# Performance work log

Hardware: AMD Instinct MI355X
Metric: run time of the kernel (lower is better)

Reference implementation:

```python
import jax, jax.numpy as jnp
import numpy as np

B, S, H, NH = 8, 1024, 1024, 16
HD = H // NH  # 64


def setup_inputs() -> dict:
    key = jax.random.key(0)
    ks = jax.random.split(key, 7)
    scale = 1.0 / np.sqrt(H)
    return {
        "hidden_states": jax.random.normal(ks[0], (B, S, H), jnp.float32),
        "Wq": jax.random.normal(ks[1], (H, H), jnp.float32) * scale,
        "bq": jax.random.normal(ks[2], (H,), jnp.float32) * 0.01,
        "Wk": jax.random.normal(ks[3], (H, H), jnp.float32) * scale,
        "bk": jax.random.normal(ks[4], (H,), jnp.float32) * 0.01,
        "Wv": jax.random.normal(ks[5], (H, H), jnp.float32) * scale,
        "bv": jax.random.normal(ks[6], (H,), jnp.float32) * 0.01,
    }


def _split_heads(x):
    # [B, S, H] -> [B, NH, S, HD]
    b, s, _ = x.shape
    return x.reshape(b, s, NH, HD).transpose(0, 2, 1, 3)


def reference(hidden_states, Wq, bq, Wk, bk, Wv, bv):
    q = _split_heads(hidden_states @ Wq.T + bq)
    k = _split_heads(hidden_states @ Wk.T + bk)
    v = _split_heads(hidden_states @ Wv.T + bv)
    scale = 1.0 / np.sqrt(HD).astype(np.float32)
    # [B, NH, S, S] attention logits (module materializes this fully)
    scores = jnp.einsum('bhld,bhsd->bhls', q, k) * scale
    probs = jax.nn.softmax(scores, axis=-1)  # dropout_p=0.0 -> no dropout
    ctx = jnp.einsum('bhls,bhsd->bhld', probs, v)
    # [B, NH, S, HD] -> [B, S, H]
    ctx = ctx.transpose(0, 2, 1, 3).reshape(hidden_states.shape[0], hidden_states.shape[1], H)
    return ctx
```

## Files before the change

### kernel.cpp

```cpp
#include <hip/hip_runtime.h>
#include <hip/hip_bf16.h>
#include <stdint.h>

#define B_  8
#define S_  1024
#define H_  1024
#define NH_ 16
#define HD_ 64
#define M_  (B_*S_)

using bf16x8 = __attribute__((ext_vector_type(8))) __bf16;
using f32x4  = __attribute__((ext_vector_type(4))) float;
using f32x16 = __attribute__((ext_vector_type(16))) float;
typedef int iv2 __attribute__((ext_vector_type(2)));

#define LOG2E 1.4426950408889634f

#if __has_builtin(__builtin_amdgcn_exp2f)
#define EXP2(x) __builtin_amdgcn_exp2f(x)
#else
#define EXP2(x) exp2f(x)
#endif

__device__ __forceinline__ void gload_lds16(const void* g, void* l) {
  __builtin_amdgcn_global_load_lds(
      (const __attribute__((address_space(1))) unsigned int*)g,
      (__attribute__((address_space(3))) unsigned int*)l, 16, 0, 0);
}

__device__ __forceinline__ unsigned pack_bf16(float lo, float hi) {
  unsigned r;
  asm("v_cvt_pk_bf16_f32 %0, %1, %2" : "=v"(r) : "v"(lo), "v"(hi));
  return r;
}

__device__ __forceinline__ void swapl32(unsigned& a, unsigned& b) {
#if __has_builtin(__builtin_amdgcn_permlane32_swap)
  iv2 r = __builtin_amdgcn_permlane32_swap((int)a, (int)b, false, false);
  a = (unsigned)r[0];
  b = (unsigned)r[1];
#else
  unsigned axc = (unsigned)__shfl_xor((int)a, 32);
  unsigned bxc = (unsigned)__shfl_xor((int)b, 32);
  int lane = threadIdx.x & 63;
  unsigned an = (lane < 32) ? a : bxc;
  unsigned bn = (lane < 32) ? axc : b;
  a = an; b = bn;
#endif
}

__global__ void __launch_bounds__(256) cast_bf16_kernel(const float* __restrict__ in,
                                                        __bf16* __restrict__ out, int n8) {
  int i = blockIdx.x * blockDim.x + threadIdx.x;
  int stride = gridDim.x * blockDim.x;
  for (; i < n8; i += stride) {
    float4 f0 = ((const float4*)in)[2 * i];
    float4 f1 = ((const float4*)in)[2 * i + 1];
    bf16x8 o;
    o[0] = (__bf16)f0.x; o[1] = (__bf16)f0.y; o[2] = (__bf16)f0.z; o[3] = (__bf16)f0.w;
    o[4] = (__bf16)f1.x; o[5] = (__bf16)f1.y; o[6] = (__bf16)f1.z; o[7] = (__bf16)f1.w;
    ((bf16x8*)out)[i] = o;
  }
}

__global__ void __launch_bounds__(256) qkv_gemm_kernel(
    const __bf16* __restrict__ X,
    const __bf16* __restrict__ Wq, const __bf16* __restrict__ Wk, const __bf16* __restrict__ Wv,
    const float* __restrict__ bq, const float* __restrict__ bk, const float* __restrict__ bv,
    __bf16* __restrict__ Qo, __bf16* __restrict__ Ko, __bf16* __restrict__ Vto) {
  __shared__ __align__(16) char Asm[128 * 128];
  __shared__ __align__(16) char Bsm[128 * 128];

  const int tid = threadIdx.x;
  const int lane = tid & 63, w = tid >> 6;
  const int l15 = lane & 15, g = lane >> 4;
  const int wr = w >> 1, wc = w & 1;
  const int m0 = blockIdx.x * 128;
  const int n0 = blockIdx.y * 128;
  const int z = blockIdx.z;
  const __bf16* W = (z == 0) ? Wq : ((z == 1) ? Wk : Wv);
  const float* bias = (z == 0) ? bq : ((z == 1) ? bk : bv);

  f32x4 acc[4][4] = {};

  for (int kt = 0; kt < H_; kt += 64) {
    __syncthreads();
#pragma unroll
    for (int is = 0; is < 4; ++is) {
      int q = is * 4096 + tid * 16;
      int row = q >> 7;
      int inrow = (q & 127) ^ ((row & 7) << 4);
      const char* ga = (const char*)X + (size_t)(m0 + row) * (H_ * 2) + kt * 2 + inrow;
      const char* gb = (const char*)W + (size_t)(n0 + row) * (H_ * 2) + kt * 2 + inrow;
      gload_lds16(ga, Asm + is * 4096 + w * 1024);
      gload_lds16(gb, Bsm + is * 4096 + w * 1024);
    }
    __syncthreads();
#pragma unroll
    for (int ks = 0; ks < 2; ++ks) {
      bf16x8 a[4], b[4];
#pragma unroll
      for (int i = 0; i < 4; ++i) {
        int row = wr * 64 + i * 16 + l15;
        int chunk = (g + ks * 4) ^ (row & 7);
        a[i] = *reinterpret_cast<const bf16x8*>(Asm + row * 128 + chunk * 16);
      }
#pragma unroll
      for (int j = 0; j < 4; ++j) {
        int row = wc * 64 + j * 16 + l15;
        int chunk = (g + ks * 4) ^ (row & 7);
        b[j] = *reinterpret_cast<const bf16x8*>(Bsm + row * 128 + chunk * 16);
      }
#pragma unroll
      for (int i = 0; i < 4; ++i)
#pragma unroll
        for (int j = 0; j < 4; ++j)
          acc[i][j] = __builtin_amdgcn_mfma_f32_16x16x32_bf16(a[i], b[j], acc[i][j], 0, 0, 0);
    }
  }

#pragma unroll
  for (int i = 0; i < 4; ++i) {
#pragma unroll
    for (int j = 0; j < 4; ++j) {
      int n = n0 + wc * 64 + j * 16 + l15;
      float bs = bias[n];
      int nh = n >> 6, d = n & 63;
#pragma unroll
      for (int r = 0; r < 4; ++r) {
        int m = m0 + wr * 64 + i * 16 + 4 * g + r;
        int bb = m >> 10, s = m & 1023;
        float v = acc[i][j][r] + bs;
        if (z == 0) {
          Qo[(((size_t)bb * NH_ + nh) * S_ + s) * HD_ + d] = (__bf16)(v * (0.125f * LOG2E));
        } else if (z == 1) {
          Ko[(((size_t)bb * NH_ + nh) * S_ + s) * HD_ + d] = (__bf16)v;
        } else {
          Vto[(((size_t)bb * NH_ + nh) * HD_ + d) * S_ + s] = (__bf16)v;
        }
      }
    }
  }
}

#define CROW(r, hi) (((r) & 3) + 8 * ((r) >> 2) + 4 * (hi))

__global__ void __launch_bounds__(512) attn_kernel(
    const __bf16* __restrict__ Q,
    const __bf16* __restrict__ K,
    const __bf16* __restrict__ Vt,
    float* __restrict__ Out) {
  __shared__ __align__(16) char Ksm[8192];
  __shared__ __align__(16) char Vsm[8192];
  __shared__ __align__(16) float stat_lds[512];

  const int tid = threadIdx.x, lane = tid & 63, w = tid >> 6;
  const int l31 = lane & 31, hi = lane >> 5;
  const int head = blockIdx.y;
  const int bb = head >> 4, nh = head & 15;
  const int qw = blockIdx.x * 256 + w * 32;

  const char* Qh = (const char*)(Q + (size_t)head * S_ * HD_);
  const char* Kh = (const char*)(K + (size_t)head * S_ * HD_);
  const char* Vh = (const char*)(Vt + (size_t)head * S_ * HD_);

  bf16x8 qf[4];
#pragma unroll
  for (int slot = 0; slot < 4; ++slot)
    qf[slot] = *reinterpret_cast<const bf16x8*>(
        Qh + (size_t)(qw + l31) * 128 + slot * 32 + hi * 16);

  float m_run = -1e30f, l_run = 0.0f;
  f32x16 accO[2] = {};

  for (int kv = 0; kv < S_; kv += 64) {
    __syncthreads();
    {
      int q = tid * 16;
      int row = q >> 7;
      int inrow = (q & 127) ^ ((row & 7) << 4);
      gload_lds16(Kh + (size_t)(kv + row) * 128 + inrow, Ksm + w * 1024);
      gload_lds16(Vh + (size_t)row * 2048 + kv * 2 + inrow, Vsm + w * 1024);
    }
    __syncthreads();

    f32x16 s0 = {}, s1 = {};
#pragma unroll
    for (int slot = 0; slot < 4; ++slot) {
      int c0 = slot * 2 + hi;
      int r0 = l31;
      bf16x8 k0 = *reinterpret_cast<const bf16x8*>(Ksm + r0 * 128 + ((c0 ^ (r0 & 7)) << 4));
      int r1 = 32 + l31;
      bf16x8 k1 = *reinterpret_cast<const bf16x8*>(Ksm + r1 * 128 + ((c0 ^ (r1 & 7)) << 4));
      s0 = __builtin_amdgcn_mfma_f32_32x32x16_bf16(k0, qf[slot], s0, 0, 0, 0);
      s1 = __builtin_amdgcn_mfma_f32_32x32x16_bf16(k1, qf[slot], s1, 0, 0, 0);
    }

    float mx = -1e30f;
#pragma unroll
    for (int r = 0; r < 16; ++r) mx = fmaxf(mx, fmaxf(s0[r], s1[r]));
    mx = fmaxf(mx, __shfl_xor(mx, 32));
    float mnew = fmaxf(m_run, mx);
    float corr = EXP2(m_run - mnew);
    float sum = 0.0f;
#pragma unroll
    for (int r = 0; r < 16; ++r) {
      float p0 = EXP2(s0[r] - mnew); s0[r] = p0; sum += p0;
      float p1 = EXP2(s1[r] - mnew); s1[r] = p1; sum += p1;
    }
    sum += __shfl_xor(sum, 32);
    l_run = l_run * corr + sum;
    m_run = mnew;

    stat_lds[w * 64 + lane] = corr;
    f32x4 c4[4];
#pragma unroll
    for (int rq = 0; rq < 4; ++rq)
      c4[rq] = *reinterpret_cast<const f32x4*>(&stat_lds[w * 64 + rq * 8 + hi * 4]);
#pragma unroll
    for (int r = 0; r < 16; ++r) {
      float cr = c4[r >> 2][r & 3];
      accO[0][r] *= cr;
      accO[1][r] *= cr;
    }

    bf16x8 pa[4];
#define BUILD_PA(T, rb)                                                     \
    {                                                                       \
      unsigned x1 = pack_bf16(T[rb + 0], T[rb + 1]);                        \
      unsigned x2 = pack_bf16(T[rb + 2], T[rb + 3]);                        \
      unsigned y1 = pack_bf16(T[rb + 4], T[rb + 5]);                        \
      unsigned y2 = pack_bf16(T[rb + 6], T[rb + 7]);                        \
      swapl32(x1, y1);                                                      \
      swapl32(x2, y2);                                                      \
      union { unsigned u[4]; bf16x8 v; } cvt;                               \
      cvt.u[0] = x1; cvt.u[1] = x2; cvt.u[2] = y1; cvt.u[3] = y2;           \
      pa_out = cvt.v;                                                       \
    }
    {
      bf16x8 pa_out;
      BUILD_PA(s0, 0) pa[0] = pa_out;
      BUILD_PA(s0, 8) pa[1] = pa_out;
      BUILD_PA(s1, 0) pa[2] = pa_out;
      BUILD_PA(s1, 8) pa[3] = pa_out;
    }

#pragma unroll
    for (int ks = 0; ks < 4; ++ks) {
#pragma unroll
      for (int dt = 0; dt < 2; ++dt) {
        int rd = dt * 32 + l31;
        int ck = ks * 2 + hi;
        bf16x8 vb = *reinterpret_cast<const bf16x8*>(Vsm + rd * 128 + ((ck ^ (rd & 7)) << 4));
        accO[dt] = __builtin_amdgcn_mfma_f32_32x32x16_bf16(pa[ks], vb, accO[dt], 0, 0, 0);
      }
    }
  }

  stat_lds[w * 64 + lane] = 1.0f / l_run;
  f32x4 li4[4];
#pragma unroll
  for (int rq = 0; rq < 4; ++rq)
    li4[rq] = *reinterpret_cast<const f32x4*>(&stat_lds[w * 64 + rq * 8 + hi * 4]);

  float* Ob = Out + (size_t)bb * S_ * H_ + (size_t)nh * HD_;
#pragma unroll
  for (int r = 0; r < 16; ++r) {
    int qabs = qw + CROW(r, hi);
    float li = li4[r >> 2][r & 3];
#pragma unroll
    for (int dt = 0; dt < 2; ++dt) {
      int d = dt * 32 + l31;
      Ob[(size_t)qabs * H_ + d] = accO[dt][r] * li;
    }
  }
}

extern "C" void kernel_launch(void* const* d_in, const int* in_sizes, int n_in,
                              void* d_out, int out_size, void* d_ws, size_t ws_size,
                              hipStream_t stream) {
  const float* hs = (const float*)d_in[0];
  const float* Wq = (const float*)d_in[1];
  const float* bq = (const float*)d_in[2];
  const float* Wk = (const float*)d_in[3];
  const float* bk = (const float*)d_in[4];
  const float* Wv = (const float*)d_in[5];
  const float* bv = (const float*)d_in[6];
  float* out = (float*)d_out;
  char* ws = (char*)d_ws;

  size_t off = 0;
  __bf16* Xb  = (__bf16*)(ws + off); off += (size_t)M_ * H_ * 2;
  __bf16* Wqb = (__bf16*)(ws + off); off += (size_t)H_ * H_ * 2;
  __bf16* Wkb = (__bf16*)(ws + off); off += (size_t)H_ * H_ * 2;
  __bf16* Wvb = (__bf16*)(ws + off); off += (size_t)H_ * H_ * 2;
  __bf16* Qb  = (__bf16*)(ws + off); off += (size_t)M_ * H_ * 2;
  __bf16* Kb  = (__bf16*)(ws + off); off += (size_t)M_ * H_ * 2;
  __bf16* Vtb = (__bf16*)(ws + off); off += (size_t)M_ * H_ * 2;

  cast_bf16_kernel<<<4096, 256, 0, stream>>>(hs, Xb, M_ * H_ / 8);
  cast_bf16_kernel<<<512, 256, 0, stream>>>(Wq, Wqb, H_ * H_ / 8);
  cast_bf16_kernel<<<512, 256, 0, stream>>>(Wk, Wkb, H_ * H_ / 8);
  cast_bf16_kernel<<<512, 256, 0, stream>>>(Wv, Wvb, H_ * H_ / 8);

  qkv_gemm_kernel<<<dim3(M_ / 128, H_ / 128, 3), 256, 0, stream>>>(
      Xb, Wqb, Wkb, Wvb, bq, bk, bv, Qb, Kb, Vtb);

  attn_kernel<<<dim3(S_ / 256, B_ * NH_), 512, 0, stream>>>(Qb, Kb, Vtb, out);
}
```

Measured before the change: 160.1 us.

## Rewrite QKV GEMM with 256x256 tiles and 4-stage LDS pipeline

Replaces the 128x128 synchronous QKV GEMM with 256x256 block tiles on 512 threads, a 4-slot LDS ring prefetching three K-tiles ahead with explicit vmcnt waits, interleaved half-tile MFMA phases with setprio, and an XCD-aware block swizzle. The goal is to hide global-load latency and raise arithmetic intensity and L2 reuse. In exchange it uses 128KB of dynamic LDS and many accumulator registers, which limits occupancy, and it depends on hand-placed waitcnt and barrier logic being correct.

```diff
diff --git a/kernel.cpp b/kernel.cpp
--- a/kernel.cpp
+++ b/kernel.cpp
@@ -21,6 +21,9 @@
 #else
 #define EXP2(x) exp2f(x)
 #endif
+
+#define SBAR() asm volatile("s_barrier" ::: "memory")
+#define WAITV(n) asm volatile("s_waitcnt vmcnt(" #n ")" ::: "memory")
 
 __device__ __forceinline__ void gload_lds16(const void* g, void* l) {
   __builtin_amdgcn_global_load_lds(
@@ -63,80 +66,149 @@
   }
 }
 
-__global__ void __launch_bounds__(256) qkv_gemm_kernel(
+#define NTILE 32
+#define ASLOT(s) (lds + (size_t)(s) * 16384)
+#define BSLOT(s) (lds + 65536 + (size_t)(s) * 16384)
+
+__global__ void __launch_bounds__(512, 2) qkv_gemm_kernel(
     const __bf16* __restrict__ X,
     const __bf16* __restrict__ Wq, const __bf16* __restrict__ Wk, const __bf16* __restrict__ Wv,
     const float* __restrict__ bq, const float* __restrict__ bk, const float* __restrict__ bv,
     __bf16* __restrict__ Qo, __bf16* __restrict__ Ko, __bf16* __restrict__ Vto) {
-  __shared__ __align__(16) char Asm[128 * 128];
-  __shared__ __align__(16) char Bsm[128 * 128];
+  extern __shared__ char lds[];
 
   const int tid = threadIdx.x;
   const int lane = tid & 63, w = tid >> 6;
   const int l15 = lane & 15, g = lane >> 4;
-  const int wr = w >> 1, wc = w & 1;
-  const int m0 = blockIdx.x * 128;
-  const int n0 = blockIdx.y * 128;
-  const int z = blockIdx.z;
-  const __bf16* W = (z == 0) ? Wq : ((z == 1) ? Wk : Wv);
+  const int wm = w >> 2, wn = w & 3;
+
+  const int bid = blockIdx.x;
+  const int swz = (bid & 7) * 48 + (bid >> 3);
+  const int tm = swz / 12, tn = swz % 12;
+  const int bm0 = tm * 256;
+  const int z = tn >> 2;
+  const int nz0 = (tn & 3) * 256;
+
+  const __bf16* Wz = (z == 0) ? Wq : ((z == 1) ? Wk : Wv);
   const float* bias = (z == 0) ? bq : ((z == 1) ? bk : bv);
 
-  f32x4 acc[4][4] = {};
-
-  for (int kt = 0; kt < H_; kt += 64) {
-    __syncthreads();
-#pragma unroll
-    for (int is = 0; is < 4; ++is) {
-      int q = is * 4096 + tid * 16;
-      int row = q >> 7;
-      int inrow = (q & 127) ^ ((row & 7) << 4);
-      const char* ga = (const char*)X + (size_t)(m0 + row) * (H_ * 2) + kt * 2 + inrow;
-      const char* gb = (const char*)W + (size_t)(n0 + row) * (H_ * 2) + kt * 2 + inrow;
-      gload_lds16(ga, Asm + is * 4096 + w * 1024);
-      gload_lds16(gb, Bsm + is * 4096 + w * 1024);
-    }
-    __syncthreads();
-#pragma unroll
-    for (int ks = 0; ks < 2; ++ks) {
-      bf16x8 a[4], b[4];
-#pragma unroll
-      for (int i = 0; i < 4; ++i) {
-        int row = wr * 64 + i * 16 + l15;
-        int chunk = (g + ks * 4) ^ (row & 7);
-        a[i] = *reinterpret_cast<const bf16x8*>(Asm + row * 128 + chunk * 16);
-      }
-#pragma unroll
-      for (int j = 0; j < 4; ++j) {
-        int row = wc * 64 + j * 16 + l15;
-        int chunk = (g + ks * 4) ^ (row & 7);
-        b[j] = *reinterpret_cast<const bf16x8*>(Bsm + row * 128 + chunk * 16);
-      }
-#pragma unroll
-      for (int i = 0; i < 4; ++i)
-#pragma unroll
-        for (int j = 0; j < 4; ++j)
-          acc[i][j] = __builtin_amdgcn_mfma_f32_16x16x32_bf16(a[i], b[j], acc[i][j], 0, 0, 0);
-    }
-  }
-
-#pragma unroll
-  for (int i = 0; i < 4; ++i) {
-#pragma unroll
-    for (int j = 0; j < 4; ++j) {
-      int n = n0 + wc * 64 + j * 16 + l15;
-      float bs = bias[n];
-      int nh = n >> 6, d = n & 63;
+  const int trow = tid >> 2, tc = tid & 3;
+  const int ssw = tc ^ ((trow >> 1) & 3);
+  const char* pA0 = (const char*)X + ((size_t)(bm0 + trow) * H_ + ssw * 8) * 2;
+  const char* pA1 = (const char*)X + ((size_t)(bm0 + trow + 128) * H_ + ssw * 8) * 2;
+  const char* pB0 = (const char*)Wz + ((size_t)(nz0 + trow) * H_ + ssw * 8) * 2;
+  const char* pB1 = (const char*)Wz + ((size_t)(nz0 + trow + 128) * H_ + ssw * 8) * 2;
+
+  const int sw = (l15 >> 1) & 3;
+  const int aoff = (wm * 128 + l15) * 64 + ((g ^ sw) << 4);
+  const int boff = (wn * 64 + l15) * 64 + ((g ^ sw) << 4);
+
+  f32x4 acc[8][4] = {};
+
+#pragma unroll
+  for (int t = 0; t < 3; ++t) {
+    const size_t o = (size_t)t * 64;
+    gload_lds16(pA0 + o, ASLOT(t) + w * 1024);
+    gload_lds16(pA1 + o, ASLOT(t) + 8192 + w * 1024);
+    gload_lds16(pB0 + o, BSLOT(t) + w * 1024);
+    gload_lds16(pB1 + o, BSLOT(t) + 8192 + w * 1024);
+  }
+  WAITV(8);
+  SBAR();
+
+  for (int t = 0; t < NTILE; ++t) {
+    const int s = t & 3;
+    const char* As = ASLOT(s);
+    const char* Bs = BSLOT(s);
+    const bool st = (t + 3) < NTILE;
+    const int s3 = (t + 3) & 3;
+    const size_t o3 = (size_t)(t + 3) * 64;
+
+    bf16x8 a0 = *(const bf16x8*)(As + aoff);
+    bf16x8 a1 = *(const bf16x8*)(As + aoff + 1024);
+    bf16x8 a2 = *(const bf16x8*)(As + aoff + 2048);
+    bf16x8 a3 = *(const bf16x8*)(As + aoff + 3072);
+    bf16x8 b0 = *(const bf16x8*)(Bs + boff);
+    bf16x8 b1 = *(const bf16x8*)(Bs + boff + 1024);
+    bf16x8 b2 = *(const bf16x8*)(Bs + boff + 2048);
+    bf16x8 b3 = *(const bf16x8*)(Bs + boff + 3072);
+    if (st) {
+      gload_lds16(pA0 + o3, ASLOT(s3) + w * 1024);
+      gload_lds16(pA1 + o3, ASLOT(s3) + 8192 + w * 1024);
+    }
+    SBAR();
+    __builtin_amdgcn_s_setprio(1);
+    acc[0][0] = __builtin_amdgcn_mfma_f32_16x16x32_bf16(a0, b0, acc[0][0], 0, 0, 0);
+    acc[0][1] = __builtin_amdgcn_mfma_f32_16x16x32_bf16(a0, b1, acc[0][1], 0, 0, 0);
+    acc[0][2] = __builtin_amdgcn_mfma_f32_16x16x32_bf16(a0, b2, acc[0][2], 0, 0, 0);
+    acc[0][3] = __builtin_amdgcn_mfma_f32_16x16x32_bf16(a0, b3, acc[0][3], 0, 0, 0);
+    acc[1][0] = __builtin_amdgcn_mfma_f32_16x16x32_bf16(a1, b0, acc[1][0], 0, 0, 0);
+    acc[1][1] = __builtin_amdgcn_mfma_f32_16x16x32_bf16(a1, b1, acc[1][1], 0, 0, 0);
+    acc[1][2] = __builtin_amdgcn_mfma_f32_16x16x32_bf16(a1, b2, acc[1][2], 0, 0, 0);
+    acc[1][3] = __builtin_amdgcn_mfma_f32_16x16x32_bf16(a1, b3, acc[1][3], 0, 0, 0);
+    acc[2][0] = __builtin_amdgcn_mfma_f32_16x16x32_bf16(a2, b0, acc[2][0], 0, 0, 0);
+    acc[2][1] = __builtin_amdgcn_mfma_f32_16x16x32_bf16(a2, b1, acc[2][1], 0, 0, 0);
+    acc[2][2] = __builtin_amdgcn_mfma_f32_16x16x32_bf16(a2, b2, acc[2][2], 0, 0, 0);
+    acc[2][3] = __builtin_amdgcn_mfma_f32_16x16x32_bf16(a2, b3, acc[2][3], 0, 0, 0);
+    acc[3][0] = __builtin_amdgcn_mfma_f32_16x16x32_bf16(a3, b0, acc[3][0], 0, 0, 0);
+    acc[3][1] = __builtin_amdgcn_mfma_f32_16x16x32_bf16(a3, b1, acc[3][1], 0, 0, 0);
+    acc[3][2] = __builtin_amdgcn_mfma_f32_16x16x32_bf16(a3, b2, acc[3][2], 0, 0, 0);
+    acc[3][3] = __builtin_amdgcn_mfma_f32_16x16x32_bf16(a3, b3, acc[3][3], 0, 0, 0);
+    __builtin_amdgcn_s_setprio(0);
+    SBAR();
+
+    bf16x8 a4 = *(const bf16x8*)(As + aoff + 4096);
+    bf16x8 a5 = *(const bf16x8*)(As + aoff + 5120);
+    bf16x8 a6 = *(const bf16x8*)(As + aoff + 6144);
+    bf16x8 a7 = *(const bf16x8*)(As + aoff + 7168);
+    if (st) {
+      gload_lds16(pB0 + o3, BSLOT(s3) + w * 1024);
+      gload_lds16(pB1 + o3, BSLOT(s3) + 8192 + w * 1024);
+    }
+    if (t < NTILE - 3) { WAITV(8); }
+    else if (t == NTILE - 3) { WAITV(4); }
+    else { WAITV(0); }
+    SBAR();
+    __builtin_amdgcn_s_setprio(1);
+    acc[4][0] = __builtin_amdgcn_mfma_f32_16x16x32_bf16(a4, b0, acc[4][0], 0, 0, 0);
+    acc[4][1] = __builtin_amdgcn_mfma_f32_16x16x32_bf16(a4, b1, acc[4][1], 0, 0, 0);
+    acc[4][2] = __builtin_amdgcn_mfma_f32_16x16x32_bf16(a4, b2, acc[4][2], 0, 0, 0);
+    acc[4][3] = __builtin_amdgcn_mfma_f32_16x16x32_bf16(a4, b3, acc[4][3], 0, 0, 0);
+    acc[5][0] = __builtin_amdgcn_mfma_f32_16x16x32_bf16(a5, b0, acc[5][0], 0, 0, 0);
+    acc[5][1] = __builtin_amdgcn_mfma_f32_16x16x32_bf16(a5, b1, acc[5][1], 0, 0, 0);
+    acc[5][2] = __builtin_amdgcn_mfma_f32_16x16x32_bf16(a5, b2, acc[5][2], 0, 0, 0);
+    acc[5][3] = __builtin_amdgcn_mfma_f32_16x16x32_bf16(a5, b3, acc[5][3], 0, 0, 0);
+    acc[6][0] = __builtin_amdgcn_mfma_f32_16x16x32_bf16(a6, b0, acc[6][0], 0, 0, 0);
+    acc[6][1] = __builtin_amdgcn_mfma_f32_16x16x32_bf16(a6, b1, acc[6][1], 0, 0, 0);
+    acc[6][2] = __builtin_amdgcn_mfma_f32_16x16x32_bf16(a6, b2, acc[6][2], 0, 0, 0);
+    acc[6][3] = __builtin_amdgcn_mfma_f32_16x16x32_bf16(a6, b3, acc[6][3], 0, 0, 0);
+    acc[7][0] = __builtin_amdgcn_mfma_f32_16x16x32_bf16(a7, b0, acc[7][0], 0, 0, 0);
+    acc[7][1] = __builtin_amdgcn_mfma_f32_16x16x32_bf16(a7, b1, acc[7][1], 0, 0, 0);
+    acc[7][2] = __builtin_amdgcn_mfma_f32_16x16x32_bf16(a7, b2, acc[7][2], 0, 0, 0);
+    acc[7][3] = __builtin_amdgcn_mfma_f32_16x16x32_bf16(a7, b3, acc[7][3], 0, 0, 0);
+    __builtin_amdgcn_s_setprio(0);
+    SBAR();
+  }
+
+#pragma unroll
+  for (int nf = 0; nf < 4; ++nf) {
+    const int ng = tn * 256 + wn * 64 + nf * 16 + l15;
+    const int nzn = ng & 1023;
+    const float bs = bias[nzn];
+    const int nh = nzn >> 6, d = nzn & 63;
+#pragma unroll
+    for (int mf = 0; mf < 8; ++mf) {
 #pragma unroll
       for (int r = 0; r < 4; ++r) {
-        int m = m0 + wr * 64 + i * 16 + 4 * g + r;
-        int bb = m >> 10, s = m & 1023;
-        float v = acc[i][j][r] + bs;
+        const int m = bm0 + wm * 128 + mf * 16 + 4 * g + r;
+        const int bb = m >> 10, sI = m & 1023;
+        const float v = acc[mf][nf][r] + bs;
         if (z == 0) {
-          Qo[(((size_t)bb * NH_ + nh) * S_ + s) * HD_ + d] = (__bf16)(v * (0.125f * LOG2E));
+          Qo[(((size_t)bb * NH_ + nh) * S_ + sI) * HD_ + d] = (__bf16)(v * (0.125f * LOG2E));
         } else if (z == 1) {
-          Ko[(((size_t)bb * NH_ + nh) * S_ + s) * HD_ + d] = (__bf16)v;
+          Ko[(((size_t)bb * NH_ + nh) * S_ + sI) * HD_ + d] = (__bf16)v;
         } else {
-          Vto[(((size_t)bb * NH_ + nh) * HD_ + d) * S_ + s] = (__bf16)v;
+          Vto[(((size_t)bb * NH_ + nh) * HD_ + d) * S_ + sI] = (__bf16)v;
         }
       }
     }
@@ -298,12 +370,15 @@
   __bf16* Kb  = (__bf16*)(ws + off); off += (size_t)M_ * H_ * 2;
   __bf16* Vtb = (__bf16*)(ws + off); off += (size_t)M_ * H_ * 2;
 
+  (void)hipFuncSetAttribute((const void*)qkv_gemm_kernel,
+                            hipFuncAttributeMaxDynamicSharedMemorySize, 131072);
+
   cast_bf16_kernel<<<4096, 256, 0, stream>>>(hs, Xb, M_ * H_ / 8);
   cast_bf16_kernel<<<512, 256, 0, stream>>>(Wq, Wqb, H_ * H_ / 8);
   cast_bf16_kernel<<<512, 256, 0, stream>>>(Wk, Wkb, H_ * H_ / 8);
   cast_bf16_kernel<<<512, 256, 0, stream>>>(Wv, Wvb, H_ * H_ / 8);
 
-  qkv_gemm_kernel<<<dim3(M_ / 128, H_ / 128, 3), 256, 0, stream>>>(
+  qkv_gemm_kernel<<<384, 512, 131072, stream>>>(
       Xb, Wqb, Wkb, Wvb, bq, bk, bv, Qb, Kb, Vtb);
 
   attn_kernel<<<dim3(S_ / 256, B_ * NH_), 512, 0, stream>>>(Qb, Kb, Vtb, out);
```

Result: slower. 174.7 us (+9.2%).

## Double-buffer K/V tiles in attention and merge weight cast launches

Applied to the files above, without the earlier changes.

The attention kernel now double-buffers the K and V LDS tiles, issuing the next tile's global-to-LDS loads before computing on the current one. It uses explicit vmcnt waits and raw barriers in place of two __syncthreads per iteration, and raises wave priority around the MFMA sections. The three weight cast launches are merged into one kernel that writes Wq, Wk and Wv contiguously into the workspace. This doubles attention LDS use, and correctness depends on the manual waitcnt and barrier placement.

```diff
diff --git a/kernel.cpp b/kernel.cpp
--- a/kernel.cpp
+++ b/kernel.cpp
@@ -21,6 +21,9 @@
 #else
 #define EXP2(x) exp2f(x)
 #endif
+
+#define SBAR() asm volatile("s_barrier" ::: "memory")
+#define WAITV(n) asm volatile("s_waitcnt vmcnt(" #n ")" ::: "memory")
 
 __device__ __forceinline__ void gload_lds16(const void* g, void* l) {
   __builtin_amdgcn_global_load_lds(
@@ -63,6 +66,20 @@
   }
 }
 
+__global__ void __launch_bounds__(256) cast3_bf16_kernel(
+    const float* __restrict__ s0, const float* __restrict__ s1,
+    const float* __restrict__ s2, __bf16* __restrict__ dst) {
+  int i = blockIdx.x * blockDim.x + threadIdx.x;
+  int seg = i >> 17, rem = i & 131071;
+  const float* s = (seg == 0) ? s0 : ((seg == 1) ? s1 : s2);
+  float4 f0 = ((const float4*)s)[2 * rem];
+  float4 f1 = ((const float4*)s)[2 * rem + 1];
+  bf16x8 o;
+  o[0] = (__bf16)f0.x; o[1] = (__bf16)f0.y; o[2] = (__bf16)f0.z; o[3] = (__bf16)f0.w;
+  o[4] = (__bf16)f1.x; o[5] = (__bf16)f1.y; o[6] = (__bf16)f1.z; o[7] = (__bf16)f1.w;
+  ((bf16x8*)dst)[i] = o;
+}
+
 __global__ void __launch_bounds__(256) qkv_gemm_kernel(
     const __bf16* __restrict__ X,
     const __bf16* __restrict__ Wq, const __bf16* __restrict__ Wk, const __bf16* __restrict__ Wv,
@@ -150,8 +167,8 @@
     const __bf16* __restrict__ K,
     const __bf16* __restrict__ Vt,
     float* __restrict__ Out) {
-  __shared__ __align__(16) char Ksm[8192];
-  __shared__ __align__(16) char Vsm[8192];
+  __shared__ __align__(16) char Ksm[2][8192];
+  __shared__ __align__(16) char Vsm[2][8192];
   __shared__ __align__(16) float stat_lds[512];
 
   const int tid = threadIdx.x, lane = tid & 63, w = tid >> 6;
@@ -164,6 +181,9 @@
   const char* Kh = (const char*)(K + (size_t)head * S_ * HD_);
   const char* Vh = (const char*)(Vt + (size_t)head * S_ * HD_);
 
+  const int srow = (tid * 16) >> 7;
+  const int sinrow = ((tid * 16) & 127) ^ ((srow & 7) << 4);
+
   bf16x8 qf[4];
 #pragma unroll
   for (int slot = 0; slot < 4; ++slot)
@@ -173,28 +193,38 @@
   float m_run = -1e30f, l_run = 0.0f;
   f32x16 accO[2] = {};
 
-  for (int kv = 0; kv < S_; kv += 64) {
-    __syncthreads();
-    {
-      int q = tid * 16;
-      int row = q >> 7;
-      int inrow = (q & 127) ^ ((row & 7) << 4);
-      gload_lds16(Kh + (size_t)(kv + row) * 128 + inrow, Ksm + w * 1024);
-      gload_lds16(Vh + (size_t)row * 2048 + kv * 2 + inrow, Vsm + w * 1024);
-    }
-    __syncthreads();
+  gload_lds16(Kh + (size_t)srow * 128 + sinrow, Ksm[0] + w * 1024);
+  gload_lds16(Vh + (size_t)srow * 2048 + sinrow, Vsm[0] + w * 1024);
+
+  for (int t = 0; t < 16; ++t) {
+    const int cur = t & 1;
+    if (t < 15) {
+      const int nxt = cur ^ 1;
+      const size_t kvn = (size_t)(t + 1) * 64;
+      gload_lds16(Kh + (size_t)(kvn + srow) * 128 + sinrow, Ksm[nxt] + w * 1024);
+      gload_lds16(Vh + (size_t)srow * 2048 + kvn * 2 + sinrow, Vsm[nxt] + w * 1024);
+      WAITV(2);
+    } else {
+      WAITV(0);
+    }
+    SBAR();
+
+    const char* Kc = Ksm[cur];
+    const char* Vc = Vsm[cur];
 
     f32x16 s0 = {}, s1 = {};
+    __builtin_amdgcn_s_setprio(1);
 #pragma unroll
     for (int slot = 0; slot < 4; ++slot) {
       int c0 = slot * 2 + hi;
       int r0 = l31;
-      bf16x8 k0 = *reinterpret_cast<const bf16x8*>(Ksm + r0 * 128 + ((c0 ^ (r0 & 7)) << 4));
+      bf16x8 k0 = *reinterpret_cast<const bf16x8*>(Kc + r0 * 128 + ((c0 ^ (r0 & 7)) << 4));
       int r1 = 32 + l31;
-      bf16x8 k1 = *reinterpret_cast<const bf16x8*>(Ksm + r1 * 128 + ((c0 ^ (r1 & 7)) << 4));
+      bf16x8 k1 = *reinterpret_cast<const bf16x8*>(Kc + r1 * 128 + ((c0 ^ (r1 & 7)) << 4));
       s0 = __builtin_amdgcn_mfma_f32_32x32x16_bf16(k0, qf[slot], s0, 0, 0, 0);
       s1 = __builtin_amdgcn_mfma_f32_32x32x16_bf16(k1, qf[slot], s1, 0, 0, 0);
     }
+    __builtin_amdgcn_s_setprio(0);
 
     float mx = -1e30f;
 #pragma unroll
@@ -245,16 +275,20 @@
       BUILD_PA(s1, 8) pa[3] = pa_out;
     }
 
+    __builtin_amdgcn_s_setprio(1);
 #pragma unroll
     for (int ks = 0; ks < 4; ++ks) {
 #pragma unroll
       for (int dt = 0; dt < 2; ++dt) {
         int rd = dt * 32 + l31;
         int ck = ks * 2 + hi;
-        bf16x8 vb = *reinterpret_cast<const bf16x8*>(Vsm + rd * 128 + ((ck ^ (rd & 7)) << 4));
+        bf16x8 vb = *reinterpret_cast<const bf16x8*>(Vc + rd * 128 + ((ck ^ (rd & 7)) << 4));
         accO[dt] = __builtin_amdgcn_mfma_f32_32x32x16_bf16(pa[ks], vb, accO[dt], 0, 0, 0);
       }
     }
+    __builtin_amdgcn_s_setprio(0);
+
+    SBAR();
   }
 
   stat_lds[w * 64 + lane] = 1.0f / l_run;
@@ -299,9 +333,7 @@
   __bf16* Vtb = (__bf16*)(ws + off); off += (size_t)M_ * H_ * 2;
 
   cast_bf16_kernel<<<4096, 256, 0, stream>>>(hs, Xb, M_ * H_ / 8);
-  cast_bf16_kernel<<<512, 256, 0, stream>>>(Wq, Wqb, H_ * H_ / 8);
-  cast_bf16_kernel<<<512, 256, 0, stream>>>(Wk, Wkb, H_ * H_ / 8);
-  cast_bf16_kernel<<<512, 256, 0, stream>>>(Wv, Wvb, H_ * H_ / 8);
+  cast3_bf16_kernel<<<1536, 256, 0, stream>>>(Wq, Wk, Wv, Wqb);
 
   qkv_gemm_kernel<<<dim3(M_ / 128, H_ / 128, 3), 256, 0, stream>>>(
       Xb, Wqb, Wkb, Wvb, bq, bk, bv, Qb, Kb, Vtb);
```

New measurement: 150.6 us. 1.06x faster.
